# Kernel optimization log

Hardware: AMD Instinct MI355X
Metric: run time of the kernel (lower is better)

The kernel has to match this reference:

```python
import jax, jax.numpy as jnp
import numpy as np

B, S, D = 2, 2048, 2048
H, KV = 16, 4
HD = D // H          # 128
G = H // KV          # 4
EPS = 1e-5


def _rms_norm(t, w):
    # standard RMSNorm over last dim (intended math of the module's qk norm)
    return t * jax.lax.rsqrt(jnp.mean(t * t, axis=-1, keepdims=True) + EPS) * w


def _rope(t, cos, sin):
    # t: [b, h, s, hd]; cos/sin: [s, hd]
    hd = t.shape[-1]
    t1, t2 = t[..., : hd // 2], t[..., hd // 2 :]
    rot = jnp.concatenate([-t2, t1], axis=-1)
    return t * cos[None, None] + rot * sin[None, None]


def setup_inputs() -> dict:
    key = jax.random.key(0)
    ks = jax.random.split(key, 8)
    x = jax.random.normal(ks[0], (B, S, D), dtype=jnp.float32)
    # causal mask: True = masked out
    mask = jnp.triu(jnp.ones((S, S), dtype=bool), k=1)
    # RoPE tables
    inv_freq = 1.0 / (10000.0 ** (np.arange(0, HD, 2, dtype=np.float32) / HD))
    ang = np.arange(S, dtype=np.float32)[:, None] * inv_freq[None, :]  # [S, HD/2]
    ang = np.concatenate([ang, ang], axis=-1)                          # [S, HD]
    cos = jnp.asarray(np.cos(ang))
    sin = jnp.asarray(np.sin(ang))
    sc = 1.0 / np.sqrt(D)
    W_q = jax.random.normal(ks[1], (D, D), dtype=jnp.float32) * sc
    W_k = jax.random.normal(ks[2], (KV * HD, D), dtype=jnp.float32) * sc
    W_v = jax.random.normal(ks[3], (KV * HD, D), dtype=jnp.float32) * sc
    W_o = jax.random.normal(ks[4], (D, D), dtype=jnp.float32) * sc
    q_norm_w = jnp.ones((HD,), dtype=jnp.float32)
    k_norm_w = jnp.ones((HD,), dtype=jnp.float32)
    return {"x": x, "mask": mask, "cos": cos, "sin": sin,
            "W_q": W_q, "W_k": W_k, "W_v": W_v, "W_o": W_o,
            "q_norm_w": q_norm_w, "k_norm_w": k_norm_w}


def reference(x, mask, cos, sin, W_q, W_k, W_v, W_o, q_norm_w, k_norm_w):
    b, s, d = x.shape
    q = (x @ W_q.T).reshape(b, s, H, HD).transpose(0, 2, 1, 3)   # [b,H,s,hd]
    k = (x @ W_k.T).reshape(b, s, KV, HD).transpose(0, 2, 1, 3)  # [b,KV,s,hd]
    v = (x @ W_v.T).reshape(b, s, KV, HD).transpose(0, 2, 1, 3)
    q = _rms_norm(q, q_norm_w)
    k = _rms_norm(k, k_norm_w)
    q = _rope(q, cos, sin)
    k = _rope(k, cos, sin)
    # GQA: group queries by kv head, avoid materializing expanded K/V
    qg = q.reshape(b, KV, G, s, HD)
    scores = jnp.einsum("bkgqd,bktd->bkgqt", qg, k) / jnp.sqrt(jnp.float32(HD))
    scores = jnp.where(mask[None, None, None], -jnp.inf, scores)
    att = jax.nn.softmax(scores, axis=-1)
    ctx = jnp.einsum("bkgqt,bktd->bkgqd", att, v)
    ctx = ctx.reshape(b, H, s, HD).transpose(0, 2, 1, 3).reshape(b, s, d)
    return ctx @ W_o.T
```

## Files before the change

### kernel.cpp

```cpp
#include <hip/hip_runtime.h>

typedef unsigned short u16;
typedef __bf16 bf16x8 __attribute__((ext_vector_type(8)));
typedef float f32x4 __attribute__((ext_vector_type(4)));
typedef u16 u16x8 __attribute__((ext_vector_type(8)));
typedef u16 u16x4 __attribute__((ext_vector_type(4)));

static constexpr int S_LEN  = 2048;
static constexpr int DMODEL = 2048;
static constexpr int NKV    = 4;
static constexpr int HD     = 128;

__device__ __forceinline__ u16 f2bf(float f) {
  unsigned u = __builtin_bit_cast(unsigned, f);
  u += 0x7fffu + ((u >> 16) & 1u);
  return (u16)(u >> 16);
}
__device__ __forceinline__ float bf2f(u16 h) {
  unsigned u = ((unsigned)h) << 16;
  return __builtin_bit_cast(float, u);
}
__device__ __forceinline__ bf16x8 as_bf(u16x8 v) { return __builtin_bit_cast(bf16x8, v); }

__device__ __forceinline__ u16x8 cvt8(const float* p) {
  f32x4 lo = *(const f32x4*)p;
  f32x4 hi = *(const f32x4*)(p + 4);
  u16x8 r;
#pragma unroll
  for (int j = 0; j < 4; ++j) { r[j] = f2bf(lo[j]); r[j + 4] = f2bf(hi[j]); }
  return r;
}

__device__ __forceinline__ void gld16(const u16* g, u16* l) {
  auto gp = (const __attribute__((address_space(1))) unsigned*)(unsigned long long)g;
  auto lp = (__attribute__((address_space(3))) unsigned*)(unsigned)(unsigned long long)l;
  __builtin_amdgcn_global_load_lds(gp, lp, 16, 0, 0);
}

__global__ __launch_bounds__(256) void cvt_all(
    const float* __restrict__ x,  const float* __restrict__ wq,
    const float* __restrict__ wk, const float* __restrict__ wv,
    const float* __restrict__ wo,
    u16* __restrict__ xb, u16* __restrict__ wall, u16* __restrict__ wob)
{
  const long i = (long)blockIdx.x * 256 + threadIdx.x;
  const float* src; u16* dst; long j, o;
  if (i < 1048576)      { src = x;  dst = xb;   j = i;           o = i; }
  else if (i < 1572864) { src = wq; dst = wall; j = i - 1048576; o = i - 1048576; }
  else if (i < 1703936) { src = wk; dst = wall; j = i - 1572864; o = i - 1048576; }
  else if (i < 1835008) { src = wv; dst = wall; j = i - 1703936; o = i - 1048576; }
  else                  { src = wo; dst = wob;  j = i - 1835008; o = i - 1835008; }
  *(u16x8*)(dst + o * 8) = cvt8(src + j * 8);
}

__global__ __launch_bounds__(256) void gemm_qkv(
    const u16* __restrict__ A, const u16* __restrict__ Bw,
    u16* __restrict__ Cq, u16* __restrict__ Ck, u16* __restrict__ Cv)
{
  constexpr int K = 2048;
  __shared__ u16 As[128 * 32];
  __shared__ u16 Bs[128 * 32];
  const int bx = blockIdx.x;
  const int bm = bx / 24, bn = bx % 24;
  const int tid = threadIdx.x, wave = tid >> 6, lane = tid & 63;
  const int wm = (wave & 1) << 6, wn = (wave >> 1) << 6;
  const long m0 = (long)bm << 7, n0 = (long)bn << 7;

  f32x4 acc[4][4] = {};

  const int srow = (wave << 5) + (lane >> 2);
  const int sch  = (lane & 3) << 3;
  const u16* ga = A  + (m0 + srow) * K + sch;
  const u16* gb = Bw + (n0 + srow) * K + sch;
  u16* la = As + (wave << 10);
  u16* lb = Bs + (wave << 10);
  const long rstep = (long)16 * K;

  const int fr = lane & 15, fc = (lane >> 4) << 3;

  for (int k0 = 0; k0 < K; k0 += 32) {
    __syncthreads();
    gld16(ga + k0,         la);
    gld16(ga + k0 + rstep, la + 512);
    gld16(gb + k0,         lb);
    gld16(gb + k0 + rstep, lb + 512);
    __syncthreads();
    bf16x8 af[4], bf[4];
#pragma unroll
    for (int i = 0; i < 4; ++i)
      af[i] = as_bf(*(const u16x8*)&As[(wm + (i << 4) + fr) * 32 + fc]);
#pragma unroll
    for (int i = 0; i < 4; ++i)
      bf[i] = as_bf(*(const u16x8*)&Bs[(wn + (i << 4) + fr) * 32 + fc]);
#pragma unroll
    for (int mi = 0; mi < 4; ++mi)
#pragma unroll
      for (int ni = 0; ni < 4; ++ni)
        acc[mi][ni] = __builtin_amdgcn_mfma_f32_16x16x32_bf16(af[mi], bf[ni], acc[mi][ni], 0, 0, 0);
  }

  u16* Cb; int N2; long c0;
  if (bn < 16)      { Cb = Cq; N2 = 2048; c0 = n0; }
  else if (bn < 20) { Cb = Ck; N2 = 512;  c0 = n0 - 2048; }
  else              { Cb = Cv; N2 = 512;  c0 = n0 - 2560; }

  const int er = (lane >> 4) << 2, ec = lane & 15;
#pragma unroll
  for (int mi = 0; mi < 4; ++mi)
#pragma unroll
    for (int ni = 0; ni < 4; ++ni) {
      u16* cp = Cb + (m0 + wm + (mi << 4) + er) * N2 + (c0 + wn + (ni << 4) + ec);
#pragma unroll
      for (int r = 0; r < 4; ++r)
        cp[(long)r * N2] = f2bf(acc[mi][ni][r]);
    }
}

__global__ __launch_bounds__(256) void gemm_o(
    const u16* __restrict__ A, const u16* __restrict__ Bw, float* __restrict__ C)
{
  constexpr int K = 2048, N = 2048;
  __shared__ u16 As[128 * 32];
  __shared__ u16 Bs[128 * 32];
  const int bx = blockIdx.x;
  const int bm = bx >> 4, bn = bx & 15;
  const int tid = threadIdx.x, wave = tid >> 6, lane = tid & 63;
  const int wm = (wave & 1) << 6, wn = (wave >> 1) << 6;
  const long m0 = (long)bm << 7, n0 = (long)bn << 7;

  f32x4 acc[4][4] = {};

  const int srow = (wave << 5) + (lane >> 2);
  const int sch  = (lane & 3) << 3;
  const u16* ga = A  + (m0 + srow) * K + sch;
  const u16* gb = Bw + (n0 + srow) * K + sch;
  u16* la = As + (wave << 10);
  u16* lb = Bs + (wave << 10);
  const long rstep = (long)16 * K;

  const int fr = lane & 15, fc = (lane >> 4) << 3;

  for (int k0 = 0; k0 < K; k0 += 32) {
    __syncthreads();
    gld16(ga + k0,         la);
    gld16(ga + k0 + rstep, la + 512);
    gld16(gb + k0,         lb);
    gld16(gb + k0 + rstep, lb + 512);
    __syncthreads();
    bf16x8 af[4], bf[4];
#pragma unroll
    for (int i = 0; i < 4; ++i)
      af[i] = as_bf(*(const u16x8*)&As[(wm + (i << 4) + fr) * 32 + fc]);
#pragma unroll
    for (int i = 0; i < 4; ++i)
      bf[i] = as_bf(*(const u16x8*)&Bs[(wn + (i << 4) + fr) * 32 + fc]);
#pragma unroll
    for (int mi = 0; mi < 4; ++mi)
#pragma unroll
      for (int ni = 0; ni < 4; ++ni)
        acc[mi][ni] = __builtin_amdgcn_mfma_f32_16x16x32_bf16(af[mi], bf[ni], acc[mi][ni], 0, 0, 0);
  }

  const int er = (lane >> 4) << 2, ec = lane & 15;
#pragma unroll
  for (int mi = 0; mi < 4; ++mi)
#pragma unroll
    for (int ni = 0; ni < 4; ++ni) {
      float* cp = C + (m0 + wm + (mi << 4) + er) * N + (n0 + wn + (ni << 4) + ec);
#pragma unroll
      for (int r = 0; r < 4; ++r)
        cp[(long)r * N] = acc[mi][ni][r];
    }
}

__global__ __launch_bounds__(256) void norm_rope2(
    u16* __restrict__ qb, u16* __restrict__ kb,
    const float* __restrict__ qw, const float* __restrict__ kw,
    const float* __restrict__ cosb, const float* __restrict__ sinb)
{
  const int bx = blockIdx.x;
  u16* buf; const float* w; int sshift; float scale; int row;
  if (bx < 16384) { buf = qb; w = qw; sshift = 4; scale = 0.08838834764831845f;
                    row = bx * 4 + (threadIdx.x >> 6); }
  else            { buf = kb; w = kw; sshift = 2; scale = 1.0f;
                    row = (bx - 16384) * 4 + (threadIdx.x >> 6); }
  const int lane = threadIdx.x & 63;
  const int s = (row >> sshift) & (S_LEN - 1);
  u16* p = buf + (long)row * HD;
  float t1 = bf2f(p[lane]), t2 = bf2f(p[lane + 64]);
  float ss = t1 * t1 + t2 * t2;
#pragma unroll
  for (int off = 32; off; off >>= 1) ss += __shfl_xor(ss, off);
  const float r = rsqrtf(ss * (1.0f / 128.0f) + 1e-5f);
  t1 *= r * w[lane];
  t2 *= r * w[lane + 64];
  const float* cp = cosb + s * HD;
  const float* sp = sinb + s * HD;
  const float o1 = (t1 * cp[lane]      - t2 * sp[lane])      * scale;
  const float o2 = (t2 * cp[lane + 64] + t1 * sp[lane + 64]) * scale;
  p[lane]      = f2bf(o1);
  p[lane + 64] = f2bf(o2);
}

__global__ __launch_bounds__(256) void transpose_v(const u16* __restrict__ v,
                                                   u16* __restrict__ vt)
{
  const int idx = blockIdx.x * 256 + threadIdx.x;
  const int t0  = (idx & 255) << 3;
  const int hd0 = ((idx >> 8) & 15) << 3;
  const int bkv = idx >> 12;
  const u16* vp = v + ((long)(bkv >> 2) * S_LEN + t0) * 512 + ((bkv & 3) << 7) + hd0;
  u16x8 rw[8];
#pragma unroll
  for (int c = 0; c < 8; ++c) rw[c] = *(const u16x8*)(vp + (long)c * 512);
  u16* op = vt + ((long)bkv * HD + hd0) * S_LEN + t0;
#pragma unroll
  for (int j = 0; j < 8; ++j) {
    u16x8 o;
#pragma unroll
    for (int c = 0; c < 8; ++c) o[c] = rw[c][j];
    *(u16x8*)(op + (long)j * S_LEN) = o;
  }
}

__global__ __launch_bounds__(256, 2) void flash(
    const u16* __restrict__ q, const u16* __restrict__ k,
    const u16* __restrict__ vt, u16* __restrict__ ctx)
{
  __shared__ u16 Ks[128 * 128];
  __shared__ u16 Vs[128 * 128];
  const int tid = threadIdx.x, wave = tid >> 6, lane = tid & 63;
  const int bx  = blockIdx.x;
  const int qtr = bx & 15;
  const int bh  = bx >> 4;
  const int qt  = (bx < 256) ? (15 - qtr) : qtr;
  const int b   = bh >> 4, h = bh & 15;
  const int kv  = h >> 2;
  const int q0  = qt << 7;

  const int fr = lane & 15, fhi = lane >> 4;

  bf16x8 qf[2][4];
#pragma unroll
  for (int nq = 0; nq < 2; ++nq) {
    const long s = q0 + (wave << 5) + (nq << 4) + fr;
    const u16* qp = q + ((long)b * S_LEN + s) * DMODEL + h * HD;
#pragma unroll
    for (int kb = 0; kb < 4; ++kb)
      qf[nq][kb] = as_bf(*(const u16x8*)(qp + (kb << 5) + (fhi << 3)));
  }

  f32x4 O[8][2] = {};
  float lS[2] = {0.f, 0.f};

  const u16* kbase = k + ((long)b * S_LEN) * 512 + kv * HD;
  const u16* vbase = vt + ((long)(b * NKV + kv)) * HD * S_LEN;

  for (int jt = 0; jt <= qt; ++jt) {
    const int t0 = jt << 7;
    __syncthreads();
#pragma unroll
    for (int i = 0; i < 8; ++i) {
      const int row = (wave << 5) + (i << 2) + fhi;
      const int gc  = fr ^ (row & 15);
      gld16(kbase + (long)(t0 + row) * 512 + (gc << 3),
            Ks + (((wave << 5) + (i << 2)) << 7));
      gld16(vbase + (long)row * S_LEN + t0 + (gc << 3),
            Vs + (((wave << 5) + (i << 2)) << 7));
    }
    __syncthreads();

    f32x4 Sac[8][2] = {};
#pragma unroll
    for (int mt = 0; mt < 8; ++mt) {
      const int t = (mt << 4) + fr;
      bf16x8 kf[4];
#pragma unroll
      for (int kb = 0; kb < 4; ++kb) {
        const int cc = ((kb << 2) + fhi) ^ (t & 15);
        kf[kb] = as_bf(*(const u16x8*)&Ks[t * 128 + (cc << 3)]);
      }
#pragma unroll
      for (int nq = 0; nq < 2; ++nq)
#pragma unroll
        for (int kb = 0; kb < 4; ++kb)
          Sac[mt][nq] = __builtin_amdgcn_mfma_f32_16x16x32_bf16(kf[kb], qf[nq][kb], Sac[mt][nq], 0, 0, 0);
    }

    if (jt == qt) {
#pragma unroll
      for (int mt = 0; mt < 8; ++mt)
#pragma unroll
        for (int nq = 0; nq < 2; ++nq) {
          const int qin = (wave << 5) + (nq << 4) + fr;
#pragma unroll
          for (int r = 0; r < 4; ++r)
            if ((mt << 4) + (fhi << 2) + r > qin) Sac[mt][nq][r] = -1e30f;
        }
    }

#pragma unroll
    for (int nq = 0; nq < 2; ++nq) {
      float rsum = 0.f;
#pragma unroll
      for (int mt = 0; mt < 8; ++mt)
#pragma unroll
        for (int r = 0; r < 4; ++r) {
          const float e = __expf(Sac[mt][nq][r]);
          Sac[mt][nq][r] = e;
          rsum += e;
        }
      rsum += __shfl_xor(rsum, 16);
      rsum += __shfl_xor(rsum, 32);
      lS[nq] += rsum;
    }

    __syncthreads();

#pragma unroll
    for (int nq = 0; nq < 2; ++nq) {
      const int qrow = (wave << 5) + (nq << 4) + fr;
#pragma unroll
      for (int mt = 0; mt < 8; ++mt) {
        u16x4 pk;
#pragma unroll
        for (int r = 0; r < 4; ++r) pk[r] = f2bf(Sac[mt][nq][r]);
        const int cs = ((mt << 1) + (fhi >> 1)) ^ (fr & 7);
        *(u16x4*)&Ks[qrow * 128 + (cs << 3) + ((fhi & 1) << 2)] = pk;
      }
    }
    asm volatile("" ::: "memory");

    bf16x8 pf[2][4];
#pragma unroll
    for (int nq = 0; nq < 2; ++nq) {
      const int qrow = (wave << 5) + (nq << 4) + fr;
#pragma unroll
      for (int kt = 0; kt < 4; ++kt) {
        const int cs = ((kt << 2) + fhi) ^ (fr & 7);
        pf[nq][kt] = as_bf(*(const u16x8*)&Ks[qrow * 128 + (cs << 3)]);
      }
    }
#pragma unroll
    for (int mh = 0; mh < 8; ++mh) {
      const int hd = (mh << 4) + fr;
      bf16x8 vf[4];
#pragma unroll
      for (int kt = 0; kt < 4; ++kt) {
        const int cc = ((kt << 2) + fhi) ^ (hd & 15);
        vf[kt] = as_bf(*(const u16x8*)&Vs[hd * 128 + (cc << 3)]);
      }
#pragma unroll
      for (int nq = 0; nq < 2; ++nq)
#pragma unroll
        for (int kt = 0; kt < 4; ++kt)
          O[mh][nq] = __builtin_amdgcn_mfma_f32_16x16x32_bf16(vf[kt], pf[nq][kt], O[mh][nq], 0, 0, 0);
    }
  }

#pragma unroll
  for (int nq = 0; nq < 2; ++nq) {
    const float inv = 1.0f / lS[nq];
    const long s = q0 + (wave << 5) + (nq << 4) + fr;
    u16* cp = ctx + ((long)b * S_LEN + s) * DMODEL + h * HD;
#pragma unroll
    for (int mh = 0; mh < 8; ++mh) {
      u16x4 pk;
#pragma unroll
      for (int r = 0; r < 4; ++r) pk[r] = f2bf(O[mh][nq][r] * inv);
      *(u16x4*)(cp + (mh << 4) + (fhi << 2)) = pk;
    }
  }
}

extern "C" void kernel_launch(void* const* d_in, const int* in_sizes, int n_in,
                              void* d_out, int out_size, void* d_ws, size_t ws_size,
                              hipStream_t stream) {
  const float* x    = (const float*)d_in[0];
  const float* cosb = (const float*)d_in[2];
  const float* sinb = (const float*)d_in[3];
  const float* Wq   = (const float*)d_in[4];
  const float* Wk   = (const float*)d_in[5];
  const float* Wv   = (const float*)d_in[6];
  const float* Wo   = (const float*)d_in[7];
  const float* qw   = (const float*)d_in[8];
  const float* kw   = (const float*)d_in[9];

  u16* qb  = (u16*)d_out;
  u16* xb  = qb + 8388608;
  u16* kb   = (u16*)d_ws;
  u16* vb   = kb  + 2097152;
  u16* vtb  = vb  + 2097152;
  u16* ctx  = vtb + 2097152;
  u16* wall = ctx;
  u16* wob  = ctx + 8388608;
  float* out = (float*)d_out;

  cvt_all<<<dim3(9216), dim3(256), 0, stream>>>(x, Wq, Wk, Wv, Wo, xb, wall, wob);
  gemm_qkv<<<dim3(768), dim3(256), 0, stream>>>(xb, wall, qb, kb, vb);
  norm_rope2<<<dim3(20480), dim3(256), 0, stream>>>(qb, kb, qw, kw, cosb, sinb);
  transpose_v<<<dim3(128), dim3(256), 0, stream>>>(vb, vtb);
  flash<<<dim3(512), dim3(256), 0, stream>>>(qb, kb, vtb, ctx);
  gemm_o<<<dim3(512), dim3(256), 0, stream>>>(ctx, wob, out);
}
```

Measured before the change: 338.9 us.

## Fuse Q norm/RoPE into flash, merge K prep with V transpose, widen GEMM K-tile

The Q RMSNorm and RoPE now run inside the flash kernel's Q fragment load, using lane shuffles for the row sum of squares. This removes a full read-modify-write pass over the Q buffer. The K norm/RoPE and the V transpose are merged into one launch, dropping a kernel launch. Both GEMMs now stage 64-wide K tiles with an XOR-swizzled LDS layout, which halves the number of barrier pairs per K step and is meant to avoid bank conflicts, at the cost of twice the shared memory per block.

After: 327.1 us. -3.5%, faster.

```diff
diff --git a/kernel.cpp b/kernel.cpp
--- a/kernel.cpp
+++ b/kernel.cpp
@@ -58,8 +58,8 @@
     u16* __restrict__ Cq, u16* __restrict__ Ck, u16* __restrict__ Cv)
 {
   constexpr int K = 2048;
-  __shared__ u16 As[128 * 32];
-  __shared__ u16 Bs[128 * 32];
+  __shared__ u16 As[128 * 64];
+  __shared__ u16 Bs[128 * 64];
   const int bx = blockIdx.x;
   const int bm = bx / 24, bn = bx % 24;
   const int tid = threadIdx.x, wave = tid >> 6, lane = tid & 63;
@@ -68,35 +68,45 @@
 
   f32x4 acc[4][4] = {};
 
-  const int srow = (wave << 5) + (lane >> 2);
-  const int sch  = (lane & 3) << 3;
+  const int srow = (wave << 5) + (lane >> 3);
+  const int sch  = ((lane & 7) ^ ((lane >> 3) & 7)) << 3;
   const u16* ga = A  + (m0 + srow) * K + sch;
   const u16* gb = Bw + (n0 + srow) * K + sch;
-  u16* la = As + (wave << 10);
-  u16* lb = Bs + (wave << 10);
-  const long rstep = (long)16 * K;
-
-  const int fr = lane & 15, fc = (lane >> 4) << 3;
-
-  for (int k0 = 0; k0 < K; k0 += 32) {
-    __syncthreads();
-    gld16(ga + k0,         la);
-    gld16(ga + k0 + rstep, la + 512);
-    gld16(gb + k0,         lb);
-    gld16(gb + k0 + rstep, lb + 512);
-    __syncthreads();
-    bf16x8 af[4], bf[4];
-#pragma unroll
-    for (int i = 0; i < 4; ++i)
-      af[i] = as_bf(*(const u16x8*)&As[(wm + (i << 4) + fr) * 32 + fc]);
-#pragma unroll
-    for (int i = 0; i < 4; ++i)
-      bf[i] = as_bf(*(const u16x8*)&Bs[(wn + (i << 4) + fr) * 32 + fc]);
-#pragma unroll
-    for (int mi = 0; mi < 4; ++mi)
-#pragma unroll
-      for (int ni = 0; ni < 4; ++ni)
-        acc[mi][ni] = __builtin_amdgcn_mfma_f32_16x16x32_bf16(af[mi], bf[ni], acc[mi][ni], 0, 0, 0);
+  u16* la = As + (wave << 11);
+  u16* lb = Bs + (wave << 11);
+  const long rstep = (long)8 * K;
+
+  const int fr = lane & 15, fhi = lane >> 4;
+
+  for (int k0 = 0; k0 < K; k0 += 64) {
+    __syncthreads();
+#pragma unroll
+    for (int i = 0; i < 4; ++i) {
+      gld16(ga + k0 + i * rstep, la + i * 512);
+      gld16(gb + k0 + i * rstep, lb + i * 512);
+    }
+    __syncthreads();
+#pragma unroll
+    for (int kb = 0; kb < 2; ++kb) {
+      bf16x8 af[4], bf[4];
+#pragma unroll
+      for (int i = 0; i < 4; ++i) {
+        const int row = wm + (i << 4) + fr;
+        const int cc  = (((kb << 2) + fhi) ^ (fr & 7)) << 3;
+        af[i] = as_bf(*(const u16x8*)&As[row * 64 + cc]);
+      }
+#pragma unroll
+      for (int i = 0; i < 4; ++i) {
+        const int row = wn + (i << 4) + fr;
+        const int cc  = (((kb << 2) + fhi) ^ (fr & 7)) << 3;
+        bf[i] = as_bf(*(const u16x8*)&Bs[row * 64 + cc]);
+      }
+#pragma unroll
+      for (int mi = 0; mi < 4; ++mi)
+#pragma unroll
+        for (int ni = 0; ni < 4; ++ni)
+          acc[mi][ni] = __builtin_amdgcn_mfma_f32_16x16x32_bf16(af[mi], bf[ni], acc[mi][ni], 0, 0, 0);
+    }
   }
 
   u16* Cb; int N2; long c0;
@@ -120,8 +130,8 @@
     const u16* __restrict__ A, const u16* __restrict__ Bw, float* __restrict__ C)
 {
   constexpr int K = 2048, N = 2048;
-  __shared__ u16 As[128 * 32];
-  __shared__ u16 Bs[128 * 32];
+  __shared__ u16 As[128 * 64];
+  __shared__ u16 Bs[128 * 64];
   const int bx = blockIdx.x;
   const int bm = bx >> 4, bn = bx & 15;
   const int tid = threadIdx.x, wave = tid >> 6, lane = tid & 63;
@@ -130,35 +140,39 @@
 
   f32x4 acc[4][4] = {};
 
-  const int srow = (wave << 5) + (lane >> 2);
-  const int sch  = (lane & 3) << 3;
+  const int srow = (wave << 5) + (lane >> 3);
+  const int sch  = ((lane & 7) ^ ((lane >> 3) & 7)) << 3;
   const u16* ga = A  + (m0 + srow) * K + sch;
   const u16* gb = Bw + (n0 + srow) * K + sch;
-  u16* la = As + (wave << 10);
-  u16* lb = Bs + (wave << 10);
-  const long rstep = (long)16 * K;
-
-  const int fr = lane & 15, fc = (lane >> 4) << 3;
-
-  for (int k0 = 0; k0 < K; k0 += 32) {
-    __syncthreads();
-    gld16(ga + k0,         la);
-    gld16(ga + k0 + rstep, la + 512);
-    gld16(gb + k0,         lb);
-    gld16(gb + k0 + rstep, lb + 512);
-    __syncthreads();
-    bf16x8 af[4], bf[4];
-#pragma unroll
-    for (int i = 0; i < 4; ++i)
-      af[i] = as_bf(*(const u16x8*)&As[(wm + (i << 4) + fr) * 32 + fc]);
-#pragma unroll
-    for (int i = 0; i < 4; ++i)
-      bf[i] = as_bf(*(const u16x8*)&Bs[(wn + (i << 4) + fr) * 32 + fc]);
-#pragma unroll
-    for (int mi = 0; mi < 4; ++mi)
-#pragma unroll
-      for (int ni = 0; ni < 4; ++ni)
-        acc[mi][ni] = __builtin_amdgcn_mfma_f32_16x16x32_bf16(af[mi], bf[ni], acc[mi][ni], 0, 0, 0);
+  u16* la = As + (wave << 11);
+  u16* lb = Bs + (wave << 11);
+  const long rstep = (long)8 * K;
+
+  const int fr = lane & 15, fhi = lane >> 4;
+
+  for (int k0 = 0; k0 < K; k0 += 64) {
+    __syncthreads();
+#pragma unroll
+    for (int i = 0; i < 4; ++i) {
+      gld16(ga + k0 + i * rstep, la + i * 512);
+      gld16(gb + k0 + i * rstep, lb + i * 512);
+    }
+    __syncthreads();
+#pragma unroll
+    for (int kb = 0; kb < 2; ++kb) {
+      bf16x8 af[4], bf[4];
+#pragma unroll
+      for (int i = 0; i < 4; ++i) {
+        const int cc = (((kb << 2) + fhi) ^ (fr & 7)) << 3;
+        af[i] = as_bf(*(const u16x8*)&As[(wm + (i << 4) + fr) * 64 + cc]);
+        bf[i] = as_bf(*(const u16x8*)&Bs[(wn + (i << 4) + fr) * 64 + cc]);
+      }
+#pragma unroll
+      for (int mi = 0; mi < 4; ++mi)
+#pragma unroll
+        for (int ni = 0; ni < 4; ++ni)
+          acc[mi][ni] = __builtin_amdgcn_mfma_f32_16x16x32_bf16(af[mi], bf[ni], acc[mi][ni], 0, 0, 0);
+    }
   }
 
   const int er = (lane >> 4) << 2, ec = lane & 15;
@@ -173,59 +187,53 @@
     }
 }
 
-__global__ __launch_bounds__(256) void norm_rope2(
-    u16* __restrict__ qb, u16* __restrict__ kb,
-    const float* __restrict__ qw, const float* __restrict__ kw,
-    const float* __restrict__ cosb, const float* __restrict__ sinb)
+__global__ __launch_bounds__(256) void k_prep(
+    u16* __restrict__ kb, const float* __restrict__ kw,
+    const float* __restrict__ cosb, const float* __restrict__ sinb,
+    const u16* __restrict__ v, u16* __restrict__ vt)
 {
   const int bx = blockIdx.x;
-  u16* buf; const float* w; int sshift; float scale; int row;
-  if (bx < 16384) { buf = qb; w = qw; sshift = 4; scale = 0.08838834764831845f;
-                    row = bx * 4 + (threadIdx.x >> 6); }
-  else            { buf = kb; w = kw; sshift = 2; scale = 1.0f;
-                    row = (bx - 16384) * 4 + (threadIdx.x >> 6); }
-  const int lane = threadIdx.x & 63;
-  const int s = (row >> sshift) & (S_LEN - 1);
-  u16* p = buf + (long)row * HD;
-  float t1 = bf2f(p[lane]), t2 = bf2f(p[lane + 64]);
-  float ss = t1 * t1 + t2 * t2;
-#pragma unroll
-  for (int off = 32; off; off >>= 1) ss += __shfl_xor(ss, off);
-  const float r = rsqrtf(ss * (1.0f / 128.0f) + 1e-5f);
-  t1 *= r * w[lane];
-  t2 *= r * w[lane + 64];
-  const float* cp = cosb + s * HD;
-  const float* sp = sinb + s * HD;
-  const float o1 = (t1 * cp[lane]      - t2 * sp[lane])      * scale;
-  const float o2 = (t2 * cp[lane + 64] + t1 * sp[lane + 64]) * scale;
-  p[lane]      = f2bf(o1);
-  p[lane + 64] = f2bf(o2);
-}
-
-__global__ __launch_bounds__(256) void transpose_v(const u16* __restrict__ v,
-                                                   u16* __restrict__ vt)
-{
-  const int idx = blockIdx.x * 256 + threadIdx.x;
-  const int t0  = (idx & 255) << 3;
-  const int hd0 = ((idx >> 8) & 15) << 3;
-  const int bkv = idx >> 12;
-  const u16* vp = v + ((long)(bkv >> 2) * S_LEN + t0) * 512 + ((bkv & 3) << 7) + hd0;
-  u16x8 rw[8];
-#pragma unroll
-  for (int c = 0; c < 8; ++c) rw[c] = *(const u16x8*)(vp + (long)c * 512);
-  u16* op = vt + ((long)bkv * HD + hd0) * S_LEN + t0;
-#pragma unroll
-  for (int j = 0; j < 8; ++j) {
-    u16x8 o;
-#pragma unroll
-    for (int c = 0; c < 8; ++c) o[c] = rw[c][j];
-    *(u16x8*)(op + (long)j * S_LEN) = o;
+  if (bx < 4096) {
+    const int row  = bx * 4 + (threadIdx.x >> 6);
+    const int lane = threadIdx.x & 63;
+    const int s = (row >> 2) & (S_LEN - 1);
+    u16* p = kb + (long)row * HD;
+    float t1 = bf2f(p[lane]), t2 = bf2f(p[lane + 64]);
+    float ss = t1 * t1 + t2 * t2;
+#pragma unroll
+    for (int off = 32; off; off >>= 1) ss += __shfl_xor(ss, off);
+    const float r = rsqrtf(ss * (1.0f / 128.0f) + 1e-5f);
+    t1 *= r * kw[lane];
+    t2 *= r * kw[lane + 64];
+    const float* cp = cosb + s * HD;
+    const float* sp = sinb + s * HD;
+    p[lane]      = f2bf(t1 * cp[lane]      - t2 * sp[lane]);
+    p[lane + 64] = f2bf(t2 * cp[lane + 64] + t1 * sp[lane + 64]);
+  } else {
+    const int idx = (bx - 4096) * 256 + threadIdx.x;
+    const int t0  = (idx & 255) << 3;
+    const int hd0 = ((idx >> 8) & 15) << 3;
+    const int bkv = idx >> 12;
+    const u16* vp = v + ((long)(bkv >> 2) * S_LEN + t0) * 512 + ((bkv & 3) << 7) + hd0;
+    u16x8 rw[8];
+#pragma unroll
+    for (int c = 0; c < 8; ++c) rw[c] = *(const u16x8*)(vp + (long)c * 512);
+    u16* op = vt + ((long)bkv * HD + hd0) * S_LEN + t0;
+#pragma unroll
+    for (int j = 0; j < 8; ++j) {
+      u16x8 o;
+#pragma unroll
+      for (int c = 0; c < 8; ++c) o[c] = rw[c][j];
+      *(u16x8*)(op + (long)j * S_LEN) = o;
+    }
   }
 }
 
 __global__ __launch_bounds__(256, 2) void flash(
     const u16* __restrict__ q, const u16* __restrict__ k,
-    const u16* __restrict__ vt, u16* __restrict__ ctx)
+    const u16* __restrict__ vt, u16* __restrict__ ctx,
+    const float* __restrict__ qw,
+    const float* __restrict__ cosb, const float* __restrict__ sinb)
 {
   __shared__ u16 Ks[128 * 128];
   __shared__ u16 Vs[128 * 128];
@@ -243,11 +251,39 @@
   bf16x8 qf[2][4];
 #pragma unroll
   for (int nq = 0; nq < 2; ++nq) {
-    const long s = q0 + (wave << 5) + (nq << 4) + fr;
-    const u16* qp = q + ((long)b * S_LEN + s) * DMODEL + h * HD;
-#pragma unroll
-    for (int kb = 0; kb < 4; ++kb)
-      qf[nq][kb] = as_bf(*(const u16x8*)(qp + (kb << 5) + (fhi << 3)));
+    const int srow = q0 + (wave << 5) + (nq << 4) + fr;
+    const u16* qp = q + ((long)b * S_LEN + srow) * DMODEL + h * HD;
+    float qv[4][8];
+    float ss = 0.f;
+#pragma unroll
+    for (int kb = 0; kb < 4; ++kb) {
+      u16x8 raw = *(const u16x8*)(qp + (kb << 5) + (fhi << 3));
+#pragma unroll
+      for (int j = 0; j < 8; ++j) {
+        const float v = bf2f(raw[j]);
+        qv[kb][j] = v;
+        ss += v * v;
+      }
+    }
+    ss += __shfl_xor(ss, 16);
+    ss += __shfl_xor(ss, 32);
+    const float rn = rsqrtf(ss * (1.0f / 128.0f) + 1e-5f);
+    const float* cp = cosb + srow * HD;
+    const float* sp = sinb + srow * HD;
+#pragma unroll
+    for (int kb = 0; kb < 4; ++kb) {
+      u16x8 pk;
+#pragma unroll
+      for (int j = 0; j < 8; ++j) {
+        const int kk = (kb << 5) + (fhi << 3) + j;
+        const float tk = qv[kb][j]     * rn * qw[kk];
+        const float tp = qv[kb ^ 2][j] * rn * qw[kk ^ 64];
+        const float o = (tk * cp[kk] + ((kb < 2) ? -tp : tp) * sp[kk])
+                        * 0.08838834764831845f;
+        pk[j] = f2bf(o);
+      }
+      qf[nq][kb] = as_bf(pk);
+    }
   }
 
   f32x4 O[8][2] = {};
@@ -398,8 +434,7 @@
 
   cvt_all<<<dim3(9216), dim3(256), 0, stream>>>(x, Wq, Wk, Wv, Wo, xb, wall, wob);
   gemm_qkv<<<dim3(768), dim3(256), 0, stream>>>(xb, wall, qb, kb, vb);
-  norm_rope2<<<dim3(20480), dim3(256), 0, stream>>>(qb, kb, qw, kw, cosb, sinb);
-  transpose_v<<<dim3(128), dim3(256), 0, stream>>>(vb, vtb);
-  flash<<<dim3(512), dim3(256), 0, stream>>>(qb, kb, vtb, ctx);
+  k_prep<<<dim3(4224), dim3(256), 0, stream>>>(kb, kw, cosb, sinb, vb, vtb);
+  flash<<<dim3(512), dim3(256), 0, stream>>>(qb, kb, vtb, ctx, qw, cosb, sinb);
   gemm_o<<<dim3(512), dim3(256), 0, stream>>>(ctx, wob, out);
 }
```
